# Kernel optimization log

Measured on AMD Instinct MI355X. Metric: run time of the kernel, lower is better.

The kernel has to match this reference:

```python
import jax, jax.numpy as jnp
import numpy as np

SCALING = 16.0 / 8.0  # alpha / rank
GAMMA = 1.0
EPS = 1e-12


def setup_inputs() -> dict:
    key = jax.random.key(0)
    ks = jax.random.split(key, 8)
    B, T, H, O = 4, 2048, 4096, 4096
    E_tot, E_act, r = 16, 4, 8
    return {
        "x": jax.random.normal(ks[0], (B, T, H), jnp.float32),
        "W_base": jax.random.normal(ks[1], (O, H), jnp.float32) * 0.02,
        "b_base": jax.random.normal(ks[2], (O,), jnp.float32) * 0.02,
        "lora_A": jax.random.normal(ks[3], (E_tot, r, H), jnp.float32) * 0.02,
        "lora_B": jax.random.normal(ks[4], (E_tot, O, r), jnp.float32) * 0.02,
        "router_W": jax.random.normal(ks[5], (E_tot, H), jnp.float32) * 0.02,
        "router_b": jax.random.normal(ks[6], (E_tot,), jnp.float32) * 0.02,
        "domain_prior": jax.random.uniform(ks[7], (E_tot,), jnp.float32),
        "active": jnp.arange(E_act, dtype=jnp.int32),
    }


def reference(x, W_base, b_base, lora_A, lora_B, router_W, router_b, domain_prior, active):
    # Base linear: [B,T,H] @ [H,O] -> [B,T,O]
    y = jnp.einsum('bth,oh->bto', x, W_base) + b_base
    # Gather active experts' low-rank factors
    A = lora_A[active]   # [E, r, H]
    Bm = lora_B[active]  # [E, O, r]
    # Grouped low-rank GEMMs (dropout is identity at inference)
    z = jnp.einsum('bth,erh->bter', x, A)            # [B,T,E,r]
    contribs = jnp.einsum('bter,eor->bteo', z, Bm) * SCALING  # [B,T,E,O]
    # Token router logits over all experts, restricted to active set
    logits = jnp.einsum('bth,eh->bte', x, router_W) + router_b  # [B,T,E_tot]
    logits = logits[..., active]                                 # [B,T,E]
    prior = domain_prior[active]                                 # [E]
    alpha = jax.nn.softmax(jnp.log(prior + EPS) + logits / GAMMA, axis=-1)  # [B,T,E]
    return y + jnp.einsum('bteo,bte->bto', contribs, alpha)
```

## Files before the change

### kernel.cpp

```cpp
#include <hip/hip_runtime.h>
#include <hip/hip_bf16.h>


typedef _Float16 f16x8 __attribute__((ext_vector_type(8)));
typedef _Float16 f16x4 __attribute__((ext_vector_type(4)));
typedef float    f32x4 __attribute__((ext_vector_type(4)));

constexpr int H  = 4096;
constexpr int O  = 4096;
constexpr int KP = 4160;
constexpr int EA = 4;
constexpr float SCALING_F = 2.0f;

typedef const __attribute__((address_space(1))) void gvoid;
typedef __attribute__((address_space(3))) void svoid;

__device__ inline void gload16(const void* g, void* s) {
  __builtin_amdgcn_global_load_lds((gvoid*)g, (svoid*)s, 16, 0, 0);
}

constexpr int WH_GROUPS = O * (KP / 8);
constexpr int VH_GROUPS = 48 * (H / 8);

__global__ __launch_bounds__(256) void convert_w_kernel(
    const float* __restrict__ W, const float* __restrict__ lora_B,
    const float* __restrict__ lora_A, const float* __restrict__ router_W,
    const int* __restrict__ active, _Float16* __restrict__ wh,
    _Float16* __restrict__ vh) {
  const int g = blockIdx.x * 256 + threadIdx.x;
  float v[8];
  _Float16* dst;
  if (g < WH_GROUPS) {
    const int o = g / 520;
    const int k = (g % 520) * 8;
    dst = wh + (size_t)o * KP + k;
    if (k < H) {
      const float* s = W + (size_t)o * H + k;
      float4 a = *(const float4*)s, b = *(const float4*)(s + 4);
      v[0] = a.x; v[1] = a.y; v[2] = a.z; v[3] = a.w;
      v[4] = b.x; v[5] = b.y; v[6] = b.z; v[7] = b.w;
    } else if (k < H + 32) {
      const int e = (k - H) >> 3;
      const float* s = lora_B + ((size_t)active[e] * O + o) * 8;
      float4 a = *(const float4*)s, b = *(const float4*)(s + 4);
      v[0] = a.x; v[1] = a.y; v[2] = a.z; v[3] = a.w;
      v[4] = b.x; v[5] = b.y; v[6] = b.z; v[7] = b.w;
    } else {
#pragma unroll
      for (int i = 0; i < 8; ++i) v[i] = 0.f;
    }
  } else {
    const int gg = g - WH_GROUPS;
    if (gg >= VH_GROUPS) return;
    const int j  = gg >> 9;
    const int k  = (gg & 511) * 8;
    dst = vh + (size_t)j * H + k;
    const float* s = nullptr;
    if (j < 32)       s = lora_A + (size_t)(active[j >> 3] * 8 + (j & 7)) * H + k;
    else if (j < 36)  s = router_W + (size_t)active[j - 32] * H + k;
    if (s) {
      float4 a = *(const float4*)s, b = *(const float4*)(s + 4);
      v[0] = a.x; v[1] = a.y; v[2] = a.z; v[3] = a.w;
      v[4] = b.x; v[5] = b.y; v[6] = b.z; v[7] = b.w;
    } else {
#pragma unroll
      for (int i = 0; i < 8; ++i) v[i] = 0.f;
    }
  }
  f16x8 h;
#pragma unroll
  for (int i = 0; i < 8; ++i) h[i] = (_Float16)v[i];
  *(f16x8*)dst = h;
}

constexpr int RT = 16;
constexpr int RW = 8;
constexpr int KSL = H / RW;

__global__ __launch_bounds__(512) void router_fused_kernel(
    const float* __restrict__ x, const _Float16* __restrict__ vh,
    const float* __restrict__ router_b, const float* __restrict__ prior,
    const int* __restrict__ active, _Float16* __restrict__ xh) {
  __shared__ float zred[RW][RT][48];
  const int tid  = threadIdx.x;
  const int lane = tid & 63;
  const int w    = tid >> 6;
  const long t0  = (long)blockIdx.x * RT;
  const int r15  = lane & 15;
  const int kg   = lane >> 4;
  const long row = t0 + r15;

  f32x4 acc[3];
  const f32x4 zero = {0.f, 0.f, 0.f, 0.f};
  acc[0] = zero; acc[1] = zero; acc[2] = zero;

  const float*    xp  = x  + row * H  + w * KSL + kg * 8;
  _Float16*       xhp = xh + row * KP + w * KSL + kg * 8;
  const _Float16* vp  = vh + (size_t)r15 * H + w * KSL + kg * 8;

#pragma unroll 4
  for (int s = 0; s < KSL / 32; ++s) {
    const int ko = s * 32;
    float4 v0 = *(const float4*)(xp + ko);
    float4 v1 = *(const float4*)(xp + ko + 4);
    f16x8 a;
    a[0] = (_Float16)v0.x; a[1] = (_Float16)v0.y;
    a[2] = (_Float16)v0.z; a[3] = (_Float16)v0.w;
    a[4] = (_Float16)v1.x; a[5] = (_Float16)v1.y;
    a[6] = (_Float16)v1.z; a[7] = (_Float16)v1.w;
    *(f16x8*)(xhp + ko) = a;
#pragma unroll
    for (int nf = 0; nf < 3; ++nf) {
      f16x8 b = *(const f16x8*)(vp + (size_t)nf * 16 * H + ko);
      acc[nf] = __builtin_amdgcn_mfma_f32_16x16x32_f16(a, b, acc[nf], 0, 0, 0);
    }
  }

#pragma unroll
  for (int nf = 0; nf < 3; ++nf)
#pragma unroll
    for (int r = 0; r < 4; ++r)
      zred[w][kg * 4 + r][nf * 16 + r15] = acc[nf][r];
  __syncthreads();

  float s0 = 0.f, s1 = 0.f;
  {
    const int a0 = tid;
    if (a0 < RT * 48) {
      const int t = a0 / 48, j = a0 % 48;
#pragma unroll
      for (int ww = 0; ww < RW; ++ww) s0 += zred[ww][t][j];
    }
    const int a1 = tid + 512;
    if (a1 < RT * 48) {
      const int t = a1 / 48, j = a1 % 48;
#pragma unroll
      for (int ww = 0; ww < RW; ++ww) s1 += zred[ww][t][j];
    }
  }
  __syncthreads();
  if (tid < RT * 48) zred[0][tid / 48][tid % 48] = s0;
  if (tid + 512 < RT * 48) zred[0][(tid + 512) / 48][(tid + 512) % 48] = s1;
  __syncthreads();

  if (tid < RT * EA) {
    const int t = tid >> 2, e = tid & 3;
    const float* zt = &zred[0][t][0];
    float le[EA], mx = -1e30f;
#pragma unroll
    for (int e2 = 0; e2 < EA; ++e2) {
      const int ae = active[e2];
      le[e2] = logf(prior[ae] + 1e-12f) + zt[32 + e2] + router_b[ae];
      mx = fmaxf(mx, le[e2]);
    }
    float sum = 0.f;
#pragma unroll
    for (int e2 = 0; e2 < EA; ++e2) sum += expf(le[e2] - mx);
    const float a = expf(le[e] - mx) / sum * SCALING_F;
    f16x8 ch;
#pragma unroll
    for (int r = 0; r < 8; ++r) ch[r] = (_Float16)(a * zt[e * 8 + r]);
    _Float16* xr = xh + (t0 + t) * KP + H;
    *(f16x8*)(xr + e * 8) = ch;
    f16x8 zz;
#pragma unroll
    for (int r = 0; r < 8; ++r) zz[r] = (_Float16)0.f;
    *(f16x8*)(xr + 32 + e * 8) = zz;
  }
}

constexpr int BM = 128, BN = 128, BK = 64;

__global__ __launch_bounds__(256) void gemm_kernel(
    const _Float16* __restrict__ xh, const _Float16* __restrict__ wh,
    const float* __restrict__ b_base, float* __restrict__ out) {
  __shared__ _Float16 As[BM * BK];
  __shared__ _Float16 Ws[BN * BK];
  const int tid  = threadIdx.x;
  const int lane = tid & 63;
  const int wave = tid >> 6;
  const int im = (int)(blockIdx.x >> 5);
  const int in = (int)(blockIdx.x & 31);
  const size_t trow0 = (size_t)im * BM;
  const size_t ocol0 = (size_t)in * BN;
  const int wr = wave >> 1, wc = wave & 1;

  f32x4 acc[4][4];
  const f32x4 zero = {0.f, 0.f, 0.f, 0.f};
#pragma unroll
  for (int m = 0; m < 4; ++m)
#pragma unroll
    for (int n = 0; n < 4; ++n) acc[m][n] = zero;

  const int srow  = lane >> 3;
  const int sslot = (lane & 7) ^ srow;
  const int r15 = lane & 15;
  const int kg  = lane >> 4;

  for (int step = 0; step < KP / BK; ++step) {
    const int k0 = step * BK;
    __syncthreads();
#pragma unroll
    for (int i = 0; i < 8; ++i) {
      const int ch  = wave + 4 * i;
      const int sub = ch & 15;
      const int row = sub * 8 + srow;
      if (ch < 16)
        gload16(xh + (trow0 + row) * KP + k0 + sslot * 8, As + sub * 512);
      else
        gload16(wh + (ocol0 + row) * KP + k0 + sslot * 8, Ws + sub * 512);
    }
    __syncthreads();
#pragma unroll
    for (int kk = 0; kk < 2; ++kk) {
      f16x8 a[4], b[4];
#pragma unroll
      for (int m = 0; m < 4; ++m) {
        const int row  = wr * 64 + m * 16 + r15;
        const int slot = (kk * 4 + kg) ^ (row & 7);
        a[m] = *(const f16x8*)(As + row * 64 + slot * 8);
      }
#pragma unroll
      for (int n = 0; n < 4; ++n) {
        const int row  = wc * 64 + n * 16 + r15;
        const int slot = (kk * 4 + kg) ^ (row & 7);
        b[n] = *(const f16x8*)(Ws + row * 64 + slot * 8);
      }
#pragma unroll
      for (int m = 0; m < 4; ++m)
#pragma unroll
        for (int n = 0; n < 4; ++n)
          acc[m][n] = __builtin_amdgcn_mfma_f32_16x16x32_f16(a[m], b[n], acc[m][n], 0, 0, 0);
    }
  }
#pragma unroll
  for (int n = 0; n < 4; ++n) {
    const size_t col = ocol0 + wc * 64 + n * 16 + r15;
    const float bb = b_base[col];
#pragma unroll
    for (int m = 0; m < 4; ++m) {
      const size_t row = trow0 + wr * 64 + m * 16 + kg * 4;
#pragma unroll
      for (int j = 0; j < 4; ++j)
        out[(row + j) * O + col] = acc[m][n][j] + bb;
    }
  }
}

extern "C" void kernel_launch(void* const* d_in, const int* in_sizes, int n_in,
                              void* d_out, int out_size, void* d_ws, size_t ws_size,
                              hipStream_t stream) {
  const float* x        = (const float*)d_in[0];
  const float* W_base   = (const float*)d_in[1];
  const float* b_base   = (const float*)d_in[2];
  const float* lora_A   = (const float*)d_in[3];
  const float* lora_B   = (const float*)d_in[4];
  const float* router_W = (const float*)d_in[5];
  const float* router_b = (const float*)d_in[6];
  const float* prior    = (const float*)d_in[7];
  const int*   active   = (const int*)d_in[8];
  float* out = (float*)d_out;

  const int M = in_sizes[0] / H;

  char* ws = (char*)d_ws;
  _Float16* xh = (_Float16*)ws;
  _Float16* wh = (_Float16*)(ws + (size_t)M * KP * 2);
  _Float16* vh = (_Float16*)(ws + (size_t)M * KP * 2 + (size_t)O * KP * 2);

  const int cw_grid = (WH_GROUPS + VH_GROUPS + 255) / 256;
  convert_w_kernel<<<cw_grid, 256, 0, stream>>>(W_base, lora_B, lora_A, router_W,
                                                active, wh, vh);
  router_fused_kernel<<<M / RT, 512, 0, stream>>>(x, vh, router_b, prior, active, xh);
  gemm_kernel<<<(M / BM) * (O / BN), 256, 0, stream>>>(xh, wh, b_base, out);
}
```

Before: 580.1 us.

## Restructure router kernel with LDS-staged tiles, row-per-block weight convert, GEMM block swizzle

The router kernel now stages fp16 x and the 48-row expert/router weight slab into swizzled LDS in 128-wide K chunks, with register prefetch of the next x chunk. Previously every lane read V fragments straight from global memory. The weight conversion kernel now gives one block per output row, and the main GEMM remaps block IDs so neighbouring blocks share weight column tiles for better L2 reuse. In exchange, the router adds two barriers per chunk and drops to 256 threads per block.

```diff
diff --git a/kernel.cpp b/kernel.cpp
--- a/kernel.cpp
+++ b/kernel.cpp
@@ -3,7 +3,6 @@
 
 
 typedef _Float16 f16x8 __attribute__((ext_vector_type(8)));
-typedef _Float16 f16x4 __attribute__((ext_vector_type(4)));
 typedef float    f32x4 __attribute__((ext_vector_type(4)));
 
 constexpr int H  = 4096;
@@ -19,101 +18,125 @@
   __builtin_amdgcn_global_load_lds((gvoid*)g, (svoid*)s, 16, 0, 0);
 }
 
-constexpr int WH_GROUPS = O * (KP / 8);
-constexpr int VH_GROUPS = 48 * (H / 8);
-
-__global__ __launch_bounds__(256) void convert_w_kernel(
+__global__ __launch_bounds__(256) void convert_w3_kernel(
     const float* __restrict__ W, const float* __restrict__ lora_B,
     const float* __restrict__ lora_A, const float* __restrict__ router_W,
     const int* __restrict__ active, _Float16* __restrict__ wh,
     _Float16* __restrict__ vh) {
-  const int g = blockIdx.x * 256 + threadIdx.x;
-  float v[8];
-  _Float16* dst;
-  if (g < WH_GROUPS) {
-    const int o = g / 520;
-    const int k = (g % 520) * 8;
-    dst = wh + (size_t)o * KP + k;
-    if (k < H) {
-      const float* s = W + (size_t)o * H + k;
-      float4 a = *(const float4*)s, b = *(const float4*)(s + 4);
-      v[0] = a.x; v[1] = a.y; v[2] = a.z; v[3] = a.w;
-      v[4] = b.x; v[5] = b.y; v[6] = b.z; v[7] = b.w;
-    } else if (k < H + 32) {
-      const int e = (k - H) >> 3;
-      const float* s = lora_B + ((size_t)active[e] * O + o) * 8;
-      float4 a = *(const float4*)s, b = *(const float4*)(s + 4);
-      v[0] = a.x; v[1] = a.y; v[2] = a.z; v[3] = a.w;
-      v[4] = b.x; v[5] = b.y; v[6] = b.z; v[7] = b.w;
-    } else {
-#pragma unroll
-      for (int i = 0; i < 8; ++i) v[i] = 0.f;
+  const int bid = blockIdx.x;
+  const int tid = threadIdx.x;
+  if (bid < O) {
+    const int o = bid;
+    const float* wrow = W + (size_t)o * H;
+    _Float16* dstrow = wh + (size_t)o * KP;
+    for (int g = tid; g < 520; g += 256) {
+      const int k = g * 8;
+      float v[8];
+      if (k < H) {
+        float4 a = *(const float4*)(wrow + k), b = *(const float4*)(wrow + k + 4);
+        v[0] = a.x; v[1] = a.y; v[2] = a.z; v[3] = a.w;
+        v[4] = b.x; v[5] = b.y; v[6] = b.z; v[7] = b.w;
+      } else if (k < H + 32) {
+        const int e = (k - H) >> 3;
+        const float* s = lora_B + ((size_t)active[e] * O + o) * 8;
+        float4 a = *(const float4*)s, b = *(const float4*)(s + 4);
+        v[0] = a.x; v[1] = a.y; v[2] = a.z; v[3] = a.w;
+        v[4] = b.x; v[5] = b.y; v[6] = b.z; v[7] = b.w;
+      } else {
+#pragma unroll
+        for (int i = 0; i < 8; ++i) v[i] = 0.f;
+      }
+      f16x8 h;
+#pragma unroll
+      for (int i = 0; i < 8; ++i) h[i] = (_Float16)v[i];
+      *(f16x8*)(dstrow + k) = h;
     }
   } else {
-    const int gg = g - WH_GROUPS;
-    if (gg >= VH_GROUPS) return;
-    const int j  = gg >> 9;
-    const int k  = (gg & 511) * 8;
-    dst = vh + (size_t)j * H + k;
-    const float* s = nullptr;
-    if (j < 32)       s = lora_A + (size_t)(active[j >> 3] * 8 + (j & 7)) * H + k;
-    else if (j < 36)  s = router_W + (size_t)active[j - 32] * H + k;
-    if (s) {
-      float4 a = *(const float4*)s, b = *(const float4*)(s + 4);
-      v[0] = a.x; v[1] = a.y; v[2] = a.z; v[3] = a.w;
-      v[4] = b.x; v[5] = b.y; v[6] = b.z; v[7] = b.w;
-    } else {
-#pragma unroll
-      for (int i = 0; i < 8; ++i) v[i] = 0.f;
-    }
-  }
-  f16x8 h;
-#pragma unroll
-  for (int i = 0; i < 8; ++i) h[i] = (_Float16)v[i];
-  *(f16x8*)dst = h;
-}
-
-constexpr int RT = 16;
-constexpr int RW = 8;
-constexpr int KSL = H / RW;
-
-__global__ __launch_bounds__(512) void router_fused_kernel(
+    const int j = bid - O;
+    const float* src = nullptr;
+    if (j < 32)      src = lora_A + (size_t)(active[j >> 3] * 8 + (j & 7)) * H;
+    else if (j < 36) src = router_W + (size_t)active[j - 32] * H;
+    _Float16* dstrow = vh + (size_t)j * H;
+    for (int g = tid; g < 512; g += 256) {
+      const int k = g * 8;
+      f16x8 h;
+      if (src) {
+        float4 a = *(const float4*)(src + k), b = *(const float4*)(src + k + 4);
+        h[0] = (_Float16)a.x; h[1] = (_Float16)a.y;
+        h[2] = (_Float16)a.z; h[3] = (_Float16)a.w;
+        h[4] = (_Float16)b.x; h[5] = (_Float16)b.y;
+        h[6] = (_Float16)b.z; h[7] = (_Float16)b.w;
+      } else {
+#pragma unroll
+        for (int i = 0; i < 8; ++i) h[i] = (_Float16)0.f;
+      }
+      *(f16x8*)(dstrow + k) = h;
+    }
+  }
+}
+
+constexpr int TM = 16, KC = 128, NCH = H / KC;
+
+__global__ __launch_bounds__(256) void router_fused3_kernel(
     const float* __restrict__ x, const _Float16* __restrict__ vh,
     const float* __restrict__ router_b, const float* __restrict__ prior,
     const int* __restrict__ active, _Float16* __restrict__ xh) {
-  __shared__ float zred[RW][RT][48];
+  __shared__ _Float16 As[TM * KC];
+  __shared__ _Float16 Vs[48 * KC];
+  __shared__ float zred[4][TM][48];
   const int tid  = threadIdx.x;
   const int lane = tid & 63;
   const int w    = tid >> 6;
-  const long t0  = (long)blockIdx.x * RT;
+  const long t0  = (long)blockIdx.x * TM;
+  const int row  = tid >> 4;
+  const int c8   = tid & 15;
   const int r15  = lane & 15;
   const int kg   = lane >> 4;
-  const long row = t0 + r15;
+
+  const float* xrow = x + (t0 + row) * H + c8 * 8;
+  _Float16*    xhrow = xh + (t0 + row) * KP + c8 * 8;
+  _Float16*    asdst = As + row * KC + (c8 ^ row) * 8;
 
   f32x4 acc[3];
   const f32x4 zero = {0.f, 0.f, 0.f, 0.f};
   acc[0] = zero; acc[1] = zero; acc[2] = zero;
 
-  const float*    xp  = x  + row * H  + w * KSL + kg * 8;
-  _Float16*       xhp = xh + row * KP + w * KSL + kg * 8;
-  const _Float16* vp  = vh + (size_t)r15 * H + w * KSL + kg * 8;
-
-#pragma unroll 4
-  for (int s = 0; s < KSL / 32; ++s) {
-    const int ko = s * 32;
-    float4 v0 = *(const float4*)(xp + ko);
-    float4 v1 = *(const float4*)(xp + ko + 4);
-    f16x8 a;
-    a[0] = (_Float16)v0.x; a[1] = (_Float16)v0.y;
-    a[2] = (_Float16)v0.z; a[3] = (_Float16)v0.w;
-    a[4] = (_Float16)v1.x; a[5] = (_Float16)v1.y;
-    a[6] = (_Float16)v1.z; a[7] = (_Float16)v1.w;
-    *(f16x8*)(xhp + ko) = a;
+  float4 xa = *(const float4*)(xrow);
+  float4 xb = *(const float4*)(xrow + 4);
+
+  for (int t = 0; t < NCH; ++t) {
+    const int k0 = t * KC;
+    float4 na, nb;
+    if (t + 1 < NCH) {
+      na = *(const float4*)(xrow + k0 + KC);
+      nb = *(const float4*)(xrow + k0 + KC + 4);
+    }
+    __syncthreads();
+    f16x8 h;
+    h[0] = (_Float16)xa.x; h[1] = (_Float16)xa.y;
+    h[2] = (_Float16)xa.z; h[3] = (_Float16)xa.w;
+    h[4] = (_Float16)xb.x; h[5] = (_Float16)xb.y;
+    h[6] = (_Float16)xb.z; h[7] = (_Float16)xb.w;
+    *(f16x8*)asdst = h;
+    *(f16x8*)(xhrow + k0) = h;
+#pragma unroll
+    for (int j = 0; j < 3; ++j) {
+      const int sv   = tid + 256 * j;
+      const int vrow = sv >> 4;
+      const int vs8  = sv & 15;
+      gload16(vh + (size_t)vrow * H + k0 + ((vs8 ^ (vrow & 15)) * 8),
+              Vs + sv * 8);
+    }
+    __syncthreads();
+    const int slot = ((w * 4 + kg) ^ r15) * 8;
+    f16x8 a = *(const f16x8*)(As + r15 * KC + slot);
 #pragma unroll
     for (int nf = 0; nf < 3; ++nf) {
-      f16x8 b = *(const f16x8*)(vp + (size_t)nf * 16 * H + ko);
+      const int vr = nf * 16 + r15;
+      f16x8 b = *(const f16x8*)(Vs + vr * KC + (((w * 4 + kg) ^ (vr & 15)) * 8));
       acc[nf] = __builtin_amdgcn_mfma_f32_16x16x32_f16(a, b, acc[nf], 0, 0, 0);
     }
+    xa = na; xb = nb;
   }
 
 #pragma unroll
@@ -123,29 +146,24 @@
       zred[w][kg * 4 + r][nf * 16 + r15] = acc[nf][r];
   __syncthreads();
 
-  float s0 = 0.f, s1 = 0.f;
-  {
-    const int a0 = tid;
-    if (a0 < RT * 48) {
-      const int t = a0 / 48, j = a0 % 48;
-#pragma unroll
-      for (int ww = 0; ww < RW; ++ww) s0 += zred[ww][t][j];
-    }
-    const int a1 = tid + 512;
-    if (a1 < RT * 48) {
-      const int t = a1 / 48, j = a1 % 48;
-#pragma unroll
-      for (int ww = 0; ww < RW; ++ww) s1 += zred[ww][t][j];
-    }
+  float s[3];
+#pragma unroll
+  for (int j = 0; j < 3; ++j) {
+    const int sl = tid + 256 * j;
+    const int tt = sl / 48, jj = sl % 48;
+    s[j] = zred[0][tt][jj] + zred[1][tt][jj] + zred[2][tt][jj] + zred[3][tt][jj];
   }
   __syncthreads();
-  if (tid < RT * 48) zred[0][tid / 48][tid % 48] = s0;
-  if (tid + 512 < RT * 48) zred[0][(tid + 512) / 48][(tid + 512) % 48] = s1;
+#pragma unroll
+  for (int j = 0; j < 3; ++j) {
+    const int sl = tid + 256 * j;
+    zred[0][sl / 48][sl % 48] = s[j];
+  }
   __syncthreads();
 
-  if (tid < RT * EA) {
-    const int t = tid >> 2, e = tid & 3;
-    const float* zt = &zred[0][t][0];
+  if (tid < TM * EA) {
+    const int tt = tid >> 2, e = tid & 3;
+    const float* zt = &zred[0][tt][0];
     float le[EA], mx = -1e30f;
 #pragma unroll
     for (int e2 = 0; e2 < EA; ++e2) {
@@ -157,14 +175,14 @@
 #pragma unroll
     for (int e2 = 0; e2 < EA; ++e2) sum += expf(le[e2] - mx);
     const float a = expf(le[e] - mx) / sum * SCALING_F;
-    f16x8 ch;
-#pragma unroll
-    for (int r = 0; r < 8; ++r) ch[r] = (_Float16)(a * zt[e * 8 + r]);
-    _Float16* xr = xh + (t0 + t) * KP + H;
+    f16x8 ch, zz;
+#pragma unroll
+    for (int r = 0; r < 8; ++r) {
+      ch[r] = (_Float16)(a * zt[e * 8 + r]);
+      zz[r] = (_Float16)0.f;
+    }
+    _Float16* xr = xh + (t0 + tt) * KP + H;
     *(f16x8*)(xr + e * 8) = ch;
-    f16x8 zz;
-#pragma unroll
-    for (int r = 0; r < 8; ++r) zz[r] = (_Float16)0.f;
     *(f16x8*)(xr + 32 + e * 8) = zz;
   }
 }
@@ -179,8 +197,10 @@
   const int tid  = threadIdx.x;
   const int lane = tid & 63;
   const int wave = tid >> 6;
-  const int im = (int)(blockIdx.x >> 5);
-  const int in = (int)(blockIdx.x & 31);
+  const int bid = (int)blockIdx.x;
+  const int swz = (bid & 7) * 256 + (bid >> 3);
+  const int im = swz >> 5;
+  const int in = swz & 31;
   const size_t trow0 = (size_t)im * BM;
   const size_t ocol0 = (size_t)in * BN;
   const int wr = wave >> 1, wc = wave & 1;
@@ -268,9 +288,8 @@
   _Float16* wh = (_Float16*)(ws + (size_t)M * KP * 2);
   _Float16* vh = (_Float16*)(ws + (size_t)M * KP * 2 + (size_t)O * KP * 2);
 
-  const int cw_grid = (WH_GROUPS + VH_GROUPS + 255) / 256;
-  convert_w_kernel<<<cw_grid, 256, 0, stream>>>(W_base, lora_B, lora_A, router_W,
+  convert_w3_kernel<<<O + 48, 256, 0, stream>>>(W_base, lora_B, lora_A, router_W,
                                                 active, wh, vh);
-  router_fused_kernel<<<M / RT, 512, 0, stream>>>(x, vh, router_b, prior, active, xh);
+  router_fused3_kernel<<<M / TM, 256, 0, stream>>>(x, vh, router_b, prior, active, xh);
   gemm_kernel<<<(M / BM) * (O / BN), 256, 0, stream>>>(xh, wh, b_base, out);
 }
```

Result: slower. 604.7 us (+4.2%).
